# Kernel tuning notes

Hardware: AMD Instinct MI355X
Metric: run time of the kernel (lower is better)

The kernel has to match this reference:

```python
import jax, jax.numpy as jnp
import numpy as np
import math

B, S, CTX, D, H, DH = 2, 2048, 256, 1024, 16, 64
INNER = H * DH
DFF = 4 * D


def layernorm(x, eps=1e-5):
    m = jnp.mean(x, axis=-1, keepdims=True)
    v = jnp.var(x, axis=-1, keepdims=True)
    return (x - m) * jax.lax.rsqrt(v + eps)


def adaln(x, t, w, b):
    # AdaLayerNorm: linear(t) -> (scale, shift); NOTE: original never applies SiLU.
    emb = t @ w + b                       # [B,1,2D]
    scale, shift = jnp.split(emb, 2, axis=-1)
    return layernorm(x) * (1.0 + scale) + shift


def mha(xq, ctx, wq, wk, wv, wo, bo):
    b, sq, _ = xq.shape
    sk = ctx.shape[1]
    q = (xq @ wq).reshape(b, sq, H, DH).transpose(0, 2, 1, 3)   # bhqd
    k = (ctx @ wk).reshape(b, sk, H, DH).transpose(0, 2, 1, 3)  # bhkd
    v = (ctx @ wv).reshape(b, sk, H, DH).transpose(0, 2, 1, 3)
    scores = jnp.einsum('bhqd,bhkd->bhqk', q, k) / math.sqrt(DH)
    attn = jax.nn.softmax(scores, axis=-1)
    out = jnp.einsum('bhqk,bhkd->bhqd', attn, v)
    out = out.transpose(0, 2, 1, 3).reshape(b, sq, INNER)
    return out @ wo + bo


def glu_ff(x, w1, b1, w2, b2):
    u = x @ w1 + b1                       # [B,S,2*DFF]
    a, gate = jnp.split(u, 2, axis=-1)
    return (a * jax.nn.gelu(gate, approximate=False)) @ w2 + b2


def setup_inputs():
    key = jax.random.key(0)
    ks = jax.random.split(key, 24)
    s = 1.0 / math.sqrt(D)

    def n(k, shape, scale=1.0):
        return jax.random.normal(k, shape, dtype=jnp.float32) * scale

    return {
        'x': n(ks[0], (B, S, D)),
        't': n(ks[1], (B, 1, D)),
        'context': n(ks[2], (B, CTX, D)),
        # self-attention (attn1)
        'attn1_wq': n(ks[3], (D, INNER), s),
        'attn1_wk': n(ks[4], (D, INNER), s),
        'attn1_wv': n(ks[5], (D, INNER), s),
        'attn1_wo': n(ks[6], (INNER, D), s),
        'attn1_bo': n(ks[7], (D,), 0.01),
        # cross-attention (attn2)
        'attn2_wq': n(ks[8], (D, INNER), s),
        'attn2_wk': n(ks[9], (D, INNER), s),
        'attn2_wv': n(ks[10], (D, INNER), s),
        'attn2_wo': n(ks[11], (INNER, D), s),
        'attn2_bo': n(ks[12], (D,), 0.01),
        # gated FFN
        'ff_w1': n(ks[13], (D, 2 * DFF), s),
        'ff_b1': n(ks[14], (2 * DFF,), 0.01),
        'ff_w2': n(ks[15], (DFF, D), 1.0 / math.sqrt(DFF)),
        'ff_b2': n(ks[16], (D,), 0.01),
        # AdaLayerNorm linears (D -> 2D)
        'norm1_w': n(ks[17], (D, 2 * D), s),
        'norm1_b': n(ks[18], (2 * D,), 0.01),
        'norm2_w': n(ks[19], (D, 2 * D), s),
        'norm2_b': n(ks[20], (2 * D,), 0.01),
        'norm3_w': n(ks[21], (D, 2 * D), s),
        'norm3_b': n(ks[22], (2 * D,), 0.01),
    }


def reference(x, t, context,
              attn1_wq, attn1_wk, attn1_wv, attn1_wo, attn1_bo,
              attn2_wq, attn2_wk, attn2_wv, attn2_wo, attn2_bo,
              ff_w1, ff_b1, ff_w2, ff_b2,
              norm1_w, norm1_b, norm2_w, norm2_b, norm3_w, norm3_b):
    h1 = adaln(x, t, norm1_w, norm1_b)
    x = mha(h1, h1, attn1_wq, attn1_wk, attn1_wv, attn1_wo, attn1_bo) + x
    h2 = adaln(x, t, norm2_w, norm2_b)
    x = mha(h2, context, attn2_wq, attn2_wk, attn2_wv, attn2_wo, attn2_bo) + x
    h3 = adaln(x, t, norm3_w, norm3_b)
    x = glu_ff(h3, ff_w1, ff_b1, ff_w2, ff_b2) + x
    return x
```

## Files before the change

### kernel.cpp

```cpp
#include <hip/hip_runtime.h>
#include <hip/hip_bf16.h>
#include <math.h>
#include <stdint.h>

typedef __bf16 bf16;
typedef __attribute__((ext_vector_type(8))) __bf16 bf16x8;
typedef __attribute__((ext_vector_type(4))) __bf16 bf16x4;
typedef __attribute__((ext_vector_type(4))) float f32x4;
typedef __attribute__((ext_vector_type(16))) float f32x16;

static constexpr int cB = 2, cS = 2048, cCTX = 256, cD = 1024, cH = 16, cDH = 64, cDFF = 4096;

__device__ __forceinline__ void glds16(const bf16* g, bf16* l) {
  __builtin_amdgcn_global_load_lds(
      (const __attribute__((address_space(1))) void*)g,
      (__attribute__((address_space(3))) void*)l, 16, 0, 0);
}

struct T8 { const float* s[8]; };
__global__ __launch_bounds__(256) void k_transpose8(T8 args, bf16* __restrict__ out) {
  __shared__ bf16 tile[64][66];
  const int n0 = blockIdx.x * 64, k0 = blockIdx.y * 64;
  const int z = blockIdx.z;
  const float* in = args.s[z];
  bf16* dst_base = out + (size_t)z * 1024 * 1024;
  const int t = threadIdx.x;
  const int r = t >> 2, cb = (t & 3) * 16;
  const float* src = in + (size_t)(k0 + r) * 1024 + n0 + cb;
#pragma unroll
  for (int q4 = 0; q4 < 4; ++q4) {
    f32x4 v = *(const f32x4*)(src + q4 * 4);
#pragma unroll
    for (int e = 0; e < 4; ++e) tile[r][cb + q4 * 4 + e] = (bf16)v[e];
  }
  __syncthreads();
  bf16* dst = dst_base + (size_t)(n0 + r) * 1024 + k0 + cb;
  bf16x8 o0, o1;
#pragma unroll
  for (int e = 0; e < 8; ++e) { o0[e] = tile[cb + e][r]; o1[e] = tile[cb + 8 + e][r]; }
  *(bf16x8*)(dst) = o0;
  *(bf16x8*)(dst + 8) = o1;
}

__global__ __launch_bounds__(256) void k_transpose(const float* __restrict__ in,
                                                   bf16* __restrict__ out, int K, int N) {
  __shared__ bf16 tile[64][66];
  const int n0 = blockIdx.x * 64, k0 = blockIdx.y * 64;
  const int t = threadIdx.x;
  const int r = t >> 2, cb = (t & 3) * 16;
  const float* src = in + (size_t)(k0 + r) * N + n0 + cb;
#pragma unroll
  for (int q4 = 0; q4 < 4; ++q4) {
    f32x4 v = *(const f32x4*)(src + q4 * 4);
#pragma unroll
    for (int e = 0; e < 4; ++e) tile[r][cb + q4 * 4 + e] = (bf16)v[e];
  }
  __syncthreads();
  bf16* dst = out + (size_t)(n0 + r) * K + k0 + cb;
  bf16x8 o0, o1;
#pragma unroll
  for (int e = 0; e < 8; ++e) { o0[e] = tile[cb + e][r]; o1[e] = tile[cb + 8 + e][r]; }
  *(bf16x8*)(dst) = o0;
  *(bf16x8*)(dst + 8) = o1;
}

__global__ __launch_bounds__(256) void k_vt(const bf16* __restrict__ V, int vstride,
                                            bf16* __restrict__ VT, int kvlen) {
  __shared__ bf16 tile[64][72];
  const int kt = blockIdx.x * 64, bh = blockIdx.y;
  const int b = bh >> 4, h = bh & 15;
  const int t = threadIdx.x, r = t >> 2, cb = (t & 3) * 16;
  const bf16* src = V + (size_t)(b * kvlen + kt + r) * vstride + h * 64 + cb;
  bf16x8 a0 = *(const bf16x8*)src;
  bf16x8 a1 = *(const bf16x8*)(src + 8);
#pragma unroll
  for (int e = 0; e < 8; ++e) { tile[r][cb + e] = a0[e]; tile[r][cb + 8 + e] = a1[e]; }
  __syncthreads();
  bf16* dst = VT + ((size_t)bh * 64 + r) * kvlen + kt + cb;
  bf16x8 o0, o1;
#pragma unroll
  for (int e = 0; e < 8; ++e) { o0[e] = tile[cb + e][r]; o1[e] = tile[cb + 8 + e][r]; }
  *(bf16x8*)(dst) = o0;
  *(bf16x8*)(dst + 8) = o1;
}

__global__ __launch_bounds__(256) void k_f2b(const float* __restrict__ in, bf16* __restrict__ out) {
  const int base = (blockIdx.x * 256 + threadIdx.x) * 4;
  f32x4 v = *(const f32x4*)(in + base);
  bf16x4 o;
#pragma unroll
  for (int e = 0; e < 4; ++e) o[e] = (bf16)v[e];
  *(bf16x4*)(out + base) = o;
}

struct EmbArgs { const float* w0; const float* w1; const float* w2;
                 const float* b0; const float* b1; const float* b2; };
__global__ __launch_bounds__(256) void k_emb3(const float* __restrict__ t, EmbArgs ea,
                                              float* __restrict__ emb) {
  const int which = blockIdx.y;
  const float* w = which == 0 ? ea.w0 : (which == 1 ? ea.w1 : ea.w2);
  const float* bias = which == 0 ? ea.b0 : (which == 1 ? ea.b1 : ea.b2);
  float* dst = emb + which * 4096;
  const int jj = threadIdx.x & 63;
  const int j = blockIdx.x * 64 + jj;
  const int kg = threadIdx.x >> 6;
  float a0 = 0.f, a1 = 0.f;
  for (int k = kg * 256; k < kg * 256 + 256; ++k) {
    float wv = w[(size_t)k * 2048 + j];
    a0 += t[k] * wv;
    a1 += t[1024 + k] * wv;
  }
  __shared__ float s0[4][64], s1[4][64];
  s0[kg][jj] = a0;
  s1[kg][jj] = a1;
  __syncthreads();
  if (threadIdx.x < 64) {
    dst[j] = s0[0][jj] + s0[1][jj] + s0[2][jj] + s0[3][jj] + bias[j];
    dst[2048 + j] = s1[0][jj] + s1[1][jj] + s1[2][jj] + s1[3][jj] + bias[j];
  }
}

__global__ __launch_bounds__(256) void k_adaln(const float* __restrict__ xres,
                                               const float* __restrict__ emb,
                                               bf16* __restrict__ h) {
  const int token = blockIdx.x;
  const int b = token >> 11;
  const float* x = xres + (size_t)token * 1024;
  const float* sc = emb + b * 2048;
  const int t = threadIdx.x;
  float v[4], s = 0.f, sq = 0.f;
#pragma unroll
  for (int i = 0; i < 4; ++i) {
    float u = x[t + 256 * i];
    v[i] = u; s += u; sq += u * u;
  }
#pragma unroll
  for (int off = 1; off < 64; off <<= 1) {
    s += __shfl_xor(s, off);
    sq += __shfl_xor(sq, off);
  }
  __shared__ float ss[4], ssq[4];
  const int wave = t >> 6;
  if ((t & 63) == 0) { ss[wave] = s; ssq[wave] = sq; }
  __syncthreads();
  const float S_ = ss[0] + ss[1] + ss[2] + ss[3];
  const float SQ = ssq[0] + ssq[1] + ssq[2] + ssq[3];
  const float mean = S_ * (1.f / 1024.f);
  const float var = SQ * (1.f / 1024.f) - mean * mean;
  const float rstd = rsqrtf(var + 1e-5f);
#pragma unroll
  for (int i = 0; i < 4; ++i) {
    const int c = t + 256 * i;
    float val = (v[i] - mean) * rstd * (1.f + sc[c]) + sc[1024 + c];
    h[(size_t)token * 1024 + c] = (bf16)val;
  }
}

template <int TN>
__global__ __launch_bounds__(256) void k_gemm_t(const bf16* __restrict__ A,
                                                const bf16* __restrict__ Bt,
                                                bf16* Cb, float* Cf,
                                                const float* __restrict__ bias,
                                                const float* res,
                                                int M, int N, int K) {
  constexpr int CJ = TN / 64;
  __shared__ bf16 As[2 * 128 * 32];
  __shared__ bf16 Bs[2 * TN * 32];
  const int m0 = blockIdx.y * 128, n0 = blockIdx.x * TN;
  const int tid = threadIdx.x;
  const int wave = tid >> 6, lane = tid & 63;
  const int l31 = lane & 31, hi8 = (lane >> 5) * 8;
  const int mw = (wave >> 1) * 64, nw = (wave & 1) * (TN / 2);
  f32x16 acc[2][CJ];
#pragma unroll
  for (int i = 0; i < 2; ++i)
#pragma unroll
    for (int j = 0; j < CJ; ++j) acc[i][j] = (f32x16)(0.f);

  const int r0 = tid >> 2, c0 = (tid & 3) << 3;
  const bf16* Ap = A + (size_t)(m0 + r0) * K + c0;
  const bf16* Bp = Bt + (size_t)(n0 + r0) * K + c0;
  bf16* lA = As + r0 * 32 + c0;
  bf16* lB = Bs + r0 * 32 + c0;

  for (int k0 = 0; k0 < K; k0 += 64) {
    __syncthreads();
    glds16(Ap + k0, lA);
    glds16(Ap + k0 + (size_t)64 * K, lA + 64 * 32);
    glds16(Ap + k0 + 32, lA + 128 * 32);
    glds16(Ap + k0 + 32 + (size_t)64 * K, lA + 192 * 32);
    glds16(Bp + k0, lB);
    if (TN == 128) glds16(Bp + k0 + (size_t)64 * K, lB + 64 * 32);
    glds16(Bp + k0 + 32, lB + TN * 32);
    if (TN == 128) glds16(Bp + k0 + 32 + (size_t)64 * K, lB + TN * 32 + 64 * 32);
    __syncthreads();
#pragma unroll
    for (int kp = 0; kp < 2; ++kp) {
      const bf16* Asp = As + kp * 128 * 32;
      const bf16* Bsp = Bs + kp * TN * 32;
#pragma unroll
      for (int kh = 0; kh < 2; ++kh) {
        bf16x8 af[2], bfr[CJ];
#pragma unroll
        for (int i = 0; i < 2; ++i)
          af[i] = *(const bf16x8*)(Asp + (mw + i * 32 + l31) * 32 + kh * 16 + hi8);
#pragma unroll
        for (int j = 0; j < CJ; ++j)
          bfr[j] = *(const bf16x8*)(Bsp + (nw + j * 32 + l31) * 32 + kh * 16 + hi8);
#pragma unroll
        for (int i = 0; i < 2; ++i)
#pragma unroll
          for (int j = 0; j < CJ; ++j)
            acc[i][j] = __builtin_amdgcn_mfma_f32_32x32x16_bf16(af[i], bfr[j], acc[i][j], 0, 0, 0);
      }
    }
  }

#pragma unroll
  for (int i = 0; i < 2; ++i) {
    const int rb = m0 + mw + i * 32 + 4 * (lane >> 5);
#pragma unroll
    for (int j = 0; j < CJ; ++j) {
      const int col = n0 + nw + j * 32 + l31;
      const float bv = bias ? bias[col] : 0.f;
#pragma unroll
      for (int reg = 0; reg < 16; ++reg) {
        const int row = rb + (reg & 3) + 8 * (reg >> 2);
        const size_t off = (size_t)row * N + col;
        float v2 = acc[i][j][reg] + bv;
        if (res) v2 += res[off];
        if (Cf) Cf[off] = v2;
        if (Cb) Cb[off] = (bf16)v2;
      }
    }
  }
}

__global__ __launch_bounds__(256) void k_gemm_glu(const bf16* __restrict__ A,
                                                  const bf16* __restrict__ Bt,
                                                  const float* __restrict__ bias,
                                                  bf16* __restrict__ Cb,
                                                  int M, int N, int K) {
  __shared__ bf16 As[2 * 128 * 32];
  __shared__ bf16 Ba[2 * 64 * 32];
  __shared__ bf16 Bg[2 * 64 * 32];
  const int m0 = blockIdx.y * 128, n0 = blockIdx.x * 64;
  const int tid = threadIdx.x;
  const int wave = tid >> 6, lane = tid & 63;
  const int l31 = lane & 31, hi8 = (lane >> 5) * 8;
  const int mw = (wave >> 1) * 64, nw = (wave & 1) * 32;
  f32x16 aa[2], ag[2];
#pragma unroll
  for (int i = 0; i < 2; ++i) { aa[i] = (f32x16)(0.f); ag[i] = (f32x16)(0.f); }

  const int r0 = tid >> 2, c0 = (tid & 3) << 3;
  const bf16* Ap = A + (size_t)(m0 + r0) * K + c0;
  const bf16* Bap = Bt + (size_t)(n0 + r0) * K + c0;
  const bf16* Bgp = Bt + (size_t)(N + n0 + r0) * K + c0;
  bf16* lA = As + r0 * 32 + c0;
  bf16* lBa = Ba + r0 * 32 + c0;
  bf16* lBg = Bg + r0 * 32 + c0;

  for (int k0 = 0; k0 < K; k0 += 64) {
    __syncthreads();
    glds16(Ap + k0, lA);
    glds16(Ap + k0 + (size_t)64 * K, lA + 64 * 32);
    glds16(Ap + k0 + 32, lA + 128 * 32);
    glds16(Ap + k0 + 32 + (size_t)64 * K, lA + 192 * 32);
    glds16(Bap + k0, lBa);
    glds16(Bap + k0 + 32, lBa + 64 * 32);
    glds16(Bgp + k0, lBg);
    glds16(Bgp + k0 + 32, lBg + 64 * 32);
    __syncthreads();
#pragma unroll
    for (int kp = 0; kp < 2; ++kp) {
      const bf16* Asp = As + kp * 128 * 32;
      const bf16* Bap_s = Ba + kp * 64 * 32;
      const bf16* Bgp_s = Bg + kp * 64 * 32;
#pragma unroll
      for (int kh = 0; kh < 2; ++kh) {
        bf16x8 af[2], ba, bg;
#pragma unroll
        for (int i = 0; i < 2; ++i)
          af[i] = *(const bf16x8*)(Asp + (mw + i * 32 + l31) * 32 + kh * 16 + hi8);
        ba = *(const bf16x8*)(Bap_s + (nw + l31) * 32 + kh * 16 + hi8);
        bg = *(const bf16x8*)(Bgp_s + (nw + l31) * 32 + kh * 16 + hi8);
#pragma unroll
        for (int i = 0; i < 2; ++i) {
          aa[i] = __builtin_amdgcn_mfma_f32_32x32x16_bf16(af[i], ba, aa[i], 0, 0, 0);
          ag[i] = __builtin_amdgcn_mfma_f32_32x32x16_bf16(af[i], bg, ag[i], 0, 0, 0);
        }
      }
    }
  }

  const int col = n0 + nw + l31;
  const float ba_v = bias[col];
  const float bg_v = bias[N + col];
#pragma unroll
  for (int i = 0; i < 2; ++i) {
    const int rb = m0 + mw + i * 32 + 4 * (lane >> 5);
#pragma unroll
    for (int reg = 0; reg < 16; ++reg) {
      const int row = rb + (reg & 3) + 8 * (reg >> 2);
      float av = aa[i][reg] + ba_v;
      float gv = ag[i][reg] + bg_v;
      float ge = 0.5f * gv * (1.0f + erff(gv * 0.70710678118654752f));
      Cb[(size_t)row * N + col] = (bf16)(av * ge);
    }
  }
}

__global__ __launch_bounds__(256) void k_attn(const bf16* __restrict__ Qp, int qstride,
                                              const bf16* __restrict__ Kp, int kstride,
                                              const bf16* __restrict__ VTp,
                                              bf16* __restrict__ Op, int kvlen) {
  const int qt = blockIdx.x * 128;
  const int hd = blockIdx.y;
  const int b = blockIdx.z;
  const int tid = threadIdx.x;
  const int wave = tid >> 6, lane = tid & 63;
  const int quad = lane >> 4, l16 = lane & 15;

  __shared__ __align__(16) bf16 Ks[64 * 64];
  __shared__ __align__(16) bf16 Vs[64 * 64];
  __shared__ __align__(16) bf16 Ps[4][32 * 72];

  bf16x8 qf[2][2];
#pragma unroll
  for (int g = 0; g < 2; ++g) {
    const bf16* qrow = Qp + (size_t)(b * cS + qt + wave * 32 + g * 16 + l16) * qstride + hd * 64;
#pragma unroll
    for (int c = 0; c < 2; ++c) {
      bf16x8 raw = *(const bf16x8*)(qrow + c * 32 + quad * 8);
#pragma unroll
      for (int e = 0; e < 8; ++e) qf[g][c][e] = (bf16)((float)raw[e] * 0.125f);
    }
  }

  float l_part[2][4] = {{0.f, 0.f, 0.f, 0.f}, {0.f, 0.f, 0.f, 0.f}};
  f32x4 o_acc[2][4];
#pragma unroll
  for (int g = 0; g < 2; ++g)
#pragma unroll
    for (int n = 0; n < 4; ++n) o_acc[g][n] = (f32x4){0.f, 0.f, 0.f, 0.f};

  const int lrow = wave * 16 + (lane >> 3);
  const int lcol = (lane & 7) * 8;
  const bf16* kbase = Kp + (size_t)(b * kvlen + lrow) * kstride + hd * 64 + lcol;
  const bf16* vbase = VTp + ((size_t)((b * 16 + hd) * 64 + lrow)) * kvlen + lcol;
  bf16* lk = Ks + lrow * 64 + lcol;
  bf16* lv = Vs + lrow * 64 + lcol;

  for (int kt = 0; kt < kvlen; kt += 64) {
    __syncthreads();
    const bf16* kg = kbase + (size_t)kt * kstride;
    glds16(kg, lk);
    glds16(kg + (size_t)8 * kstride, lk + 8 * 64);
    glds16(vbase + kt, lv);
    glds16(vbase + kt + (size_t)8 * kvlen, lv + 8 * 64);
    __syncthreads();

    f32x4 s[2][4];
#pragma unroll
    for (int g = 0; g < 2; ++g)
#pragma unroll
      for (int t = 0; t < 4; ++t) s[g][t] = (f32x4){0.f, 0.f, 0.f, 0.f};
#pragma unroll
    for (int t = 0; t < 4; ++t)
#pragma unroll
      for (int c = 0; c < 2; ++c) {
        bf16x8 kf = *(const bf16x8*)(Ks + (t * 16 + l16) * 64 + c * 32 + quad * 8);
#pragma unroll
        for (int g = 0; g < 2; ++g)
          s[g][t] = __builtin_amdgcn_mfma_f32_16x16x32_bf16(qf[g][c], kf, s[g][t], 0, 0, 0);
      }

#pragma unroll
    for (int g = 0; g < 2; ++g)
#pragma unroll
      for (int t = 0; t < 4; ++t)
#pragma unroll
        for (int r = 0; r < 4; ++r) {
          float p = __expf(s[g][t][r]);
          Ps[wave][(g * 16 + quad * 4 + r) * 72 + t * 16 + l16] = (bf16)p;
          l_part[g][r] += p;
        }

    bf16x8 pf[2][2];
#pragma unroll
    for (int g = 0; g < 2; ++g)
#pragma unroll
      for (int c = 0; c < 2; ++c)
        pf[g][c] = *(const bf16x8*)(&Ps[wave][(g * 16 + l16) * 72 + c * 32 + quad * 8]);
#pragma unroll
    for (int n = 0; n < 4; ++n)
#pragma unroll
      for (int c = 0; c < 2; ++c) {
        bf16x8 vf = *(const bf16x8*)(Vs + (n * 16 + l16) * 64 + c * 32 + quad * 8);
#pragma unroll
        for (int g = 0; g < 2; ++g)
          o_acc[g][n] = __builtin_amdgcn_mfma_f32_16x16x32_bf16(pf[g][c], vf, o_acc[g][n], 0, 0, 0);
      }
  }

#pragma unroll
  for (int g = 0; g < 2; ++g) {
    float rl[4];
#pragma unroll
    for (int r = 0; r < 4; ++r) {
      float v = l_part[g][r];
      v += __shfl_xor(v, 1);
      v += __shfl_xor(v, 2);
      v += __shfl_xor(v, 4);
      v += __shfl_xor(v, 8);
      rl[r] = 1.f / v;
    }
#pragma unroll
    for (int n = 0; n < 4; ++n)
#pragma unroll
      for (int r = 0; r < 4; ++r) {
        const int srow = qt + wave * 32 + g * 16 + quad * 4 + r;
        const int d = n * 16 + l16;
        Op[(size_t)(b * cS + srow) * 1024 + hd * 64 + d] = (bf16)(o_acc[g][n][r] * rl[r]);
      }
  }
}

extern "C" void kernel_launch(void* const* d_in, const int* in_sizes, int n_in,
                              void* d_out, int out_size, void* d_ws, size_t ws_size,
                              hipStream_t stream) {
  const float* x    = (const float*)d_in[0];
  const float* tt   = (const float*)d_in[1];
  const float* ctx  = (const float*)d_in[2];
  const float* fw1  = (const float*)d_in[13];
  const float* fb1  = (const float*)d_in[14];
  const float* fw2  = (const float*)d_in[15];
  const float* fb2  = (const float*)d_in[16];
  const float* a1bo = (const float*)d_in[7];
  const float* a2bo = (const float*)d_in[12];

  char* ws = (char*)d_ws;
  const size_t MB = 1ull << 20;
  bf16* wsq   = (bf16*)(ws + 0 * MB);
  bf16* wqkv1 = wsq;
  bf16* wto1  = (bf16*)(ws + 6 * MB);
  bf16* wtq2  = (bf16*)(ws + 8 * MB);
  bf16* wkv2w = (bf16*)(ws + 10 * MB);
  bf16* wto2  = (bf16*)(ws + 14 * MB);
  bf16* wtf1  = (bf16*)(ws + 16 * MB);
  bf16* wtf2  = (bf16*)(ws + 32 * MB);
  float* emb  = (float*)(ws + 40 * MB);
  float* emb1 = emb, *emb2 = emb + 4096, *emb3 = emb + 8192;
  bf16* ctxb  = (bf16*)(ws + 40 * MB + 262144);
  float* xres = (float*)(ws + 42 * MB);
  bf16* h     = (bf16*)(ws + 58 * MB);
  bf16* ao    = h;
  bf16* qkv   = (bf16*)(ws + 66 * MB);
  bf16* q2    = qkv;
  bf16* vT1   = (bf16*)(ws + 90 * MB);
  bf16* kv2   = (bf16*)(ws + 0 * MB);
  bf16* vT2   = (bf16*)(ws + 2 * MB);
  bf16* g     = (bf16*)(ws + 66 * MB);
  float* out  = (float*)d_out;

  const dim3 blk(256);

  T8 t8;
  t8.s[0] = (const float*)d_in[3];
  t8.s[1] = (const float*)d_in[4];
  t8.s[2] = (const float*)d_in[5];
  t8.s[3] = (const float*)d_in[6];
  t8.s[4] = (const float*)d_in[8];
  t8.s[5] = (const float*)d_in[9];
  t8.s[6] = (const float*)d_in[10];
  t8.s[7] = (const float*)d_in[11];
  k_transpose8<<<dim3(16, 16, 8), blk, 0, stream>>>(t8, wsq);
  k_transpose<<<dim3(128, 16), blk, 0, stream>>>(fw1, wtf1, 1024, 8192);
  k_transpose<<<dim3(16, 64), blk, 0, stream>>>(fw2, wtf2, 4096, 1024);

  EmbArgs ea;
  ea.w0 = (const float*)d_in[17]; ea.b0 = (const float*)d_in[18];
  ea.w1 = (const float*)d_in[19]; ea.b1 = (const float*)d_in[20];
  ea.w2 = (const float*)d_in[21]; ea.b2 = (const float*)d_in[22];
  k_emb3<<<dim3(32, 3), blk, 0, stream>>>(tt, ea, emb);
  k_f2b<<<512, blk, 0, stream>>>(ctx, ctxb);

  k_adaln<<<4096, blk, 0, stream>>>(x, emb1, h);
  k_gemm_t<128><<<dim3(24, 32), blk, 0, stream>>>(h, wqkv1, qkv, nullptr, nullptr, nullptr, 4096, 3072, 1024);
  k_vt<<<dim3(32, 32), blk, 0, stream>>>(qkv + 2048, 3072, vT1, 2048);
  k_attn<<<dim3(16, 16, 2), blk, 0, stream>>>(qkv, 3072, qkv + 1024, 3072, vT1, ao, 2048);
  k_gemm_t<64><<<dim3(16, 32), blk, 0, stream>>>(ao, wto1, nullptr, xres, a1bo, x, 4096, 1024, 1024);

  k_adaln<<<4096, blk, 0, stream>>>(xres, emb2, h);
  k_gemm_t<64><<<dim3(16, 32), blk, 0, stream>>>(h, wtq2, q2, nullptr, nullptr, nullptr, 4096, 1024, 1024);
  k_gemm_t<128><<<dim3(16, 4), blk, 0, stream>>>(ctxb, wkv2w, kv2, nullptr, nullptr, nullptr, 512, 2048, 1024);
  k_vt<<<dim3(4, 32), blk, 0, stream>>>(kv2 + 1024, 2048, vT2, 256);
  k_attn<<<dim3(16, 16, 2), blk, 0, stream>>>(q2, 1024, kv2, 2048, vT2, ao, 256);
  k_gemm_t<64><<<dim3(16, 32), blk, 0, stream>>>(ao, wto2, nullptr, xres, a2bo, xres, 4096, 1024, 1024);

  k_adaln<<<4096, blk, 0, stream>>>(xres, emb3, h);
  k_gemm_glu<<<dim3(64, 32), blk, 0, stream>>>(h, wtf1, fb1, g, 4096, 4096, 1024);
  k_gemm_t<64><<<dim3(16, 32), blk, 0, stream>>>(g, wtf2, nullptr, out, fb2, xres, 4096, 1024, 4096);
}
```

Baseline: 642.1 us.

## Rewrite GLU GEMM as 256x128 tile, 8-wave, double-buffered pipelined kernel

Replaces the FFN GLU GEMM kernel with a 512-thread kernel that computes a 256x(64 value + 64 gate) tile. It double-buffers K-halves in shared memory, interleaving async global-to-LDS loads with 16x16x32 MFMA phases under explicit barriers, waitcnts and setprio. Blocks are remapped so that each XCD owns a contiguous range of N columns, which should improve L2 reuse. The goal is to raise MFMA utilisation and hide load latency, at the cost of hardcoded shapes, high register use and fragile hand scheduling.

```diff
diff --git a/kernel.cpp b/kernel.cpp
--- a/kernel.cpp
+++ b/kernel.cpp
@@ -236,77 +236,116 @@
   }
 }
 
-__global__ __launch_bounds__(256) void k_gemm_glu(const bf16* __restrict__ A,
-                                                  const bf16* __restrict__ Bt,
-                                                  const float* __restrict__ bias,
-                                                  bf16* __restrict__ Cb,
-                                                  int M, int N, int K) {
-  __shared__ bf16 As[2 * 128 * 32];
-  __shared__ bf16 Ba[2 * 64 * 32];
-  __shared__ bf16 Bg[2 * 64 * 32];
-  const int m0 = blockIdx.y * 128, n0 = blockIdx.x * 64;
+__global__ __launch_bounds__(512, 2) void k_glu8(const bf16* __restrict__ A,
+                                                 const bf16* __restrict__ Bt,
+                                                 const float* __restrict__ bias,
+                                                 bf16* __restrict__ C) {
+  constexpr int K = 1024, NOUT = 4096, NT = K / 64, NIT = NT / 2;
+  __shared__ __align__(16) bf16 sA[2 * 2 * 8192];
+  __shared__ __align__(16) bf16 sB[2 * 2 * 8192];
+
+  const int bid = blockIdx.x;
+  const int xcd = bid & 7, bj = bid >> 3;
+  const int n_idx = xcd * 4 + (bj >> 4);
+  const int m_idx = bj & 15;
+  const int m0 = m_idx * 256, n0 = n_idx * 128;
+
   const int tid = threadIdx.x;
-  const int wave = tid >> 6, lane = tid & 63;
-  const int l31 = lane & 31, hi8 = (lane >> 5) * 8;
-  const int mw = (wave >> 1) * 64, nw = (wave & 1) * 32;
-  f32x16 aa[2], ag[2];
-#pragma unroll
-  for (int i = 0; i < 2; ++i) { aa[i] = (f32x16)(0.f); ag[i] = (f32x16)(0.f); }
-
-  const int r0 = tid >> 2, c0 = (tid & 3) << 3;
-  const bf16* Ap = A + (size_t)(m0 + r0) * K + c0;
-  const bf16* Bap = Bt + (size_t)(n0 + r0) * K + c0;
-  const bf16* Bgp = Bt + (size_t)(N + n0 + r0) * K + c0;
-  bf16* lA = As + r0 * 32 + c0;
-  bf16* lBa = Ba + r0 * 32 + c0;
-  bf16* lBg = Bg + r0 * 32 + c0;
-
-  for (int k0 = 0; k0 < K; k0 += 64) {
-    __syncthreads();
-    glds16(Ap + k0, lA);
-    glds16(Ap + k0 + (size_t)64 * K, lA + 64 * 32);
-    glds16(Ap + k0 + 32, lA + 128 * 32);
-    glds16(Ap + k0 + 32 + (size_t)64 * K, lA + 192 * 32);
-    glds16(Bap + k0, lBa);
-    glds16(Bap + k0 + 32, lBa + 64 * 32);
-    glds16(Bgp + k0, lBg);
-    glds16(Bgp + k0 + 32, lBg + 64 * 32);
-    __syncthreads();
-#pragma unroll
-    for (int kp = 0; kp < 2; ++kp) {
-      const bf16* Asp = As + kp * 128 * 32;
-      const bf16* Bap_s = Ba + kp * 64 * 32;
-      const bf16* Bgp_s = Bg + kp * 64 * 32;
-#pragma unroll
-      for (int kh = 0; kh < 2; ++kh) {
-        bf16x8 af[2], ba, bg;
-#pragma unroll
-        for (int i = 0; i < 2; ++i)
-          af[i] = *(const bf16x8*)(Asp + (mw + i * 32 + l31) * 32 + kh * 16 + hi8);
-        ba = *(const bf16x8*)(Bap_s + (nw + l31) * 32 + kh * 16 + hi8);
-        bg = *(const bf16x8*)(Bgp_s + (nw + l31) * 32 + kh * 16 + hi8);
-#pragma unroll
-        for (int i = 0; i < 2; ++i) {
-          aa[i] = __builtin_amdgcn_mfma_f32_32x32x16_bf16(af[i], ba, aa[i], 0, 0, 0);
-          ag[i] = __builtin_amdgcn_mfma_f32_32x32x16_bf16(af[i], bg, ag[i], 0, 0, 0);
-        }
+  const int wid = tid >> 6, lane = tid & 63;
+  const int l15 = lane & 15, hi = lane >> 4;
+  const int wm = wid >> 2, wn = wid & 3;
+
+  const int srA = wid * 32 + (lane >> 2);
+  const int scol = (lane & 3) * 8;
+  const bf16* aS0 = A + (size_t)(m0 + srA) * K + scol;
+  const bf16* aS1 = aS0 + (size_t)16 * K;
+  auto grow = [&](int r) {
+    return n0 + (r >> 6) * 32 + (r & 31) + ((r & 32) ? NOUT : 0);
+  };
+  const bf16* bS0 = Bt + (size_t)grow(srA) * K + scol;
+  const bf16* bS1 = Bt + (size_t)grow(srA + 16) * K + scol;
+  bf16* aD = sA + wid * 1024 + lane * 8;
+  bf16* bD = sB + wid * 1024 + lane * 8;
+  const bf16* aF = sA + (wm * 128 + l15) * 32 + hi * 8;
+  const bf16* bF = sB + (wn * 64 + l15) * 32 + hi * 8;
+
+  f32x4 acc[8][4];
+#pragma unroll
+  for (int i = 0; i < 8; ++i)
+#pragma unroll
+    for (int n = 0; n < 4; ++n) acc[i][n] = (f32x4){0.f, 0.f, 0.f, 0.f};
+  bf16x8 aq[4], bq[4];
+
+#define STG_A(bb, kh, kt) do { \
+    glds16(aS0 + (kt) * 64 + (kh) * 32, aD + ((bb) * 2 + (kh)) * 8192); \
+    glds16(aS1 + (kt) * 64 + (kh) * 32, aD + ((bb) * 2 + (kh)) * 8192 + 512); } while (0)
+#define STG_B(bb, kh, kt) do { \
+    glds16(bS0 + (kt) * 64 + (kh) * 32, bD + ((bb) * 2 + (kh)) * 8192); \
+    glds16(bS1 + (kt) * 64 + (kh) * 32, bD + ((bb) * 2 + (kh)) * 8192 + 512); } while (0)
+
+#define PH(bb, kh, mh, STAGES, VMC) do { \
+    if ((mh) == 0) { \
+      _Pragma("unroll") \
+      for (int nf = 0; nf < 4; ++nf) \
+        bq[nf] = *(const bf16x8*)(bF + ((bb) * 2 + (kh)) * 8192 + nf * 512); \
+    } \
+    _Pragma("unroll") \
+    for (int mi = 0; mi < 4; ++mi) \
+      aq[mi] = *(const bf16x8*)(aF + ((bb) * 2 + (kh)) * 8192 + ((mh) * 4 + mi) * 512); \
+    STAGES; \
+    __builtin_amdgcn_s_barrier(); \
+    asm volatile("s_waitcnt lgkmcnt(0)" ::: "memory"); \
+    __builtin_amdgcn_sched_barrier(0); \
+    __builtin_amdgcn_s_setprio(1); \
+    _Pragma("unroll") \
+    for (int mi = 0; mi < 4; ++mi) \
+      _Pragma("unroll") \
+      for (int nf = 0; nf < 4; ++nf) \
+        acc[(mh) * 4 + mi][nf] = __builtin_amdgcn_mfma_f32_16x16x32_bf16( \
+            aq[mi], bq[nf], acc[(mh) * 4 + mi][nf], 0, 0, 0); \
+    __builtin_amdgcn_s_setprio(0); \
+    VMC; \
+    __builtin_amdgcn_s_barrier(); \
+    __builtin_amdgcn_sched_barrier(0); \
+  } while (0)
+
+  STG_B(0, 0, 0); STG_A(0, 0, 0); STG_B(0, 1, 0); STG_A(0, 1, 0);
+  STG_B(1, 0, 1); STG_A(1, 0, 1); STG_B(1, 1, 1);
+  asm volatile("s_waitcnt vmcnt(6)" ::: "memory");
+  __builtin_amdgcn_s_barrier();
+  __builtin_amdgcn_sched_barrier(0);
+
+  for (int it = 0; it < NIT; ++it) {
+    const int T = 2 * it;
+    const int t2 = (T + 2 < NT) ? (T + 2) : 0;
+    const int t3 = (T + 3 < NT) ? (T + 3) : 0;
+    PH(0, 0, 0, STG_A(1, 1, T + 1), );
+    PH(0, 0, 1, STG_B(0, 0, t2), );
+    PH(0, 1, 0, STG_A(0, 0, t2), );
+    PH(0, 1, 1, STG_B(0, 1, t2), asm volatile("s_waitcnt vmcnt(6)" ::: "memory"));
+    PH(1, 0, 0, STG_A(0, 1, t2), );
+    PH(1, 0, 1, STG_B(1, 0, t3), );
+    PH(1, 1, 0, STG_A(1, 0, t3), );
+    PH(1, 1, 1, STG_B(1, 1, t3), asm volatile("s_waitcnt vmcnt(6)" ::: "memory"));
+  }
+#undef PH
+#undef STG_A
+#undef STG_B
+
+#pragma unroll
+  for (int mi = 0; mi < 8; ++mi) {
+    const int row = m0 + wm * 128 + mi * 16 + hi * 4;
+#pragma unroll
+    for (int nf = 0; nf < 2; ++nf) {
+      const int col = n0 + wn * 32 + nf * 16 + l15;
+      const float bav = bias[col], bgv = bias[NOUT + col];
+#pragma unroll
+      for (int r = 0; r < 4; ++r) {
+        float a = acc[mi][nf][r] + bav;
+        float g = acc[mi][nf + 2][r] + bgv;
+        float ge = 0.5f * g * (1.0f + erff(g * 0.70710678118654752f));
+        C[(size_t)(row + r) * NOUT + col] = (bf16)(a * ge);
       }
-    }
-  }
-
-  const int col = n0 + nw + l31;
-  const float ba_v = bias[col];
-  const float bg_v = bias[N + col];
-#pragma unroll
-  for (int i = 0; i < 2; ++i) {
-    const int rb = m0 + mw + i * 32 + 4 * (lane >> 5);
-#pragma unroll
-    for (int reg = 0; reg < 16; ++reg) {
-      const int row = rb + (reg & 3) + 8 * (reg >> 2);
-      float av = aa[i][reg] + ba_v;
-      float gv = ag[i][reg] + bg_v;
-      float ge = 0.5f * gv * (1.0f + erff(gv * 0.70710678118654752f));
-      Cb[(size_t)row * N + col] = (bf16)(av * ge);
     }
   }
 }
@@ -500,6 +539,6 @@
   k_gemm_t<64><<<dim3(16, 32), blk, 0, stream>>>(ao, wto2, nullptr, xres, a2bo, xres, 4096, 1024, 1024);
 
   k_adaln<<<4096, blk, 0, stream>>>(xres, emb3, h);
-  k_gemm_glu<<<dim3(64, 32), blk, 0, stream>>>(h, wtf1, fb1, g, 4096, 4096, 1024);
+  k_glu8<<<dim3(512), dim3(512), 0, stream>>>(h, wtf1, fb1, g);
   k_gemm_t<64><<<dim3(16, 32), blk, 0, stream>>>(g, wtf2, nullptr, out, fb2, xres, 4096, 1024, 4096);
 }
```

New measurement: 639.4 us. No clear change (-0.4%).
